# Optimization experiments

Measured on AMD Instinct MI355X. Metric: run time of the kernel, lower is better.

The kernel has to match this reference:

```python
import jax, jax.numpy as jnp
import numpy as np

D = 256   # embedding dim d; rows are d+1 = 257
N = 2048  # sequence length n; cols are n+1 = 2049
B = 16

def setup_inputs() -> dict:
    key = jax.random.key(0)
    k_h, k_p, k_q = jax.random.split(key, 3)
    H = jax.random.normal(k_h, (B, D + 1, N + 1), dtype=jnp.float32)
    P = jax.random.normal(k_p, (D + 1, D + 1), dtype=jnp.float32) * 0.01
    Q = jax.random.normal(k_q, (D + 1, D + 1), dtype=jnp.float32) * 0.01
    return {"H": H, "P": P, "Q": Q}

def reference(H, P, Q):
    # H: (B, d+1, n+1)
    n = H.shape[2] - 1
    # HtQH = H^T @ Q @ H : (B, n+1, n+1)
    HtQ = jnp.einsum('bds,de->bse', H, Q)          # (B, n+1, d+1)
    HtQH = jnp.einsum('bse,bet->bst', HtQ, H)      # (B, n+1, n+1)
    # mask M = diag(1,...,1,0): M @ HtQH zeroes the last row
    MHtQH = HtQH.at[:, -1, :].set(0.0)
    PH = jnp.einsum('de,bet->bdt', P, H)           # (B, d+1, n+1)
    attn = jnp.einsum('bds,bst->bdt', PH, MHtQH)   # (B, d+1, n+1)
    return H + attn / n
```

## Files before the change

### kernel.cpp

```cpp
#include <hip/hip_runtime.h>
#include <hip/hip_bf16.h>

#define DP     257
#define NP     2049
#define NSEQ   2048
#define NB     16
#define KLD    288
#define HROWS  320
#define TPITCH 320
#define TROWS  2176
#define KPAD   40

typedef __attribute__((ext_vector_type(8))) short bf16x8;
typedef __attribute__((ext_vector_type(4))) short bf16x4;
typedef __attribute__((ext_vector_type(4))) float f32x4;

__global__ __launch_bounds__(256) void conv_all(const float* __restrict__ H,
                                                const float* __restrict__ P,
                                                const float* __restrict__ Q,
                                                __hip_bfloat16* __restrict__ Hb,
                                                __hip_bfloat16* __restrict__ Hbt,
                                                __hip_bfloat16* __restrict__ Pb,
                                                __hip_bfloat16* __restrict__ Qt) {
    const int z  = blockIdx.z;
    const int tl = threadIdx.x & 63;
    const int er = threadIdx.x >> 6;
    __shared__ float tile[64][65];

    if (z < NB) {
        const int b  = z;
        const int t0 = blockIdx.x * 64;
        const int e0 = blockIdx.y * 64;
        const float* __restrict__ Hs = H + (size_t)b * DP * NP;
        __hip_bfloat16* __restrict__ Hbb  = Hb  + (size_t)b * HROWS * 2048;
        __hip_bfloat16* __restrict__ Hbtb = Hbt + (size_t)b * TROWS * TPITCH;

#pragma unroll
        for (int r = 0; r < 16; ++r) {
            const int el = er + r * 4;
            const int ge = e0 + el;
            const int gt = t0 + tl;
            float v = 0.f;
            if (ge < DP && gt < NP) v = Hs[(size_t)ge * NP + gt];
            tile[el][tl] = v;
            if (ge < HROWS && gt < 2048) Hbb[(size_t)ge * 2048 + gt] = __float2bfloat16(v);
        }
        __syncthreads();
#pragma unroll
        for (int r = 0; r < 16; ++r) {
            const int ttl = er + r * 4;
            const int gt = t0 + ttl;
            const int ge = e0 + tl;
            if (gt < TROWS && ge < TPITCH) {
                const float v = (ge < KLD) ? tile[tl][ttl] : 0.f;
                Hbtb[(size_t)gt * TPITCH + ge] = __float2bfloat16(v);
            }
        }
        return;
    }

    const int bx = blockIdx.x;
    if (bx >= 10) return;
    const int r0 = blockIdx.y * 64;
    if (bx < 5) {
        const int c0 = bx * 64;
#pragma unroll
        for (int r = 0; r < 16; ++r) {
            const int m = r0 + er + r * 4;
            const int k = c0 + tl;
            float v = (m < DP && k < DP) ? P[m * DP + k] : 0.f;
            if (m < KLD && k < KLD) Pb[m * KLD + k] = __float2bfloat16(v);
        }
    } else {
        const int c0 = (bx - 5) * 64;
#pragma unroll
        for (int r = 0; r < 16; ++r) {
            const int k = r0 + er + r * 4;
            const int n = c0 + tl;
            float v = (k < DP && n < DP) ? Q[k * DP + n] : 0.f;
            tile[k - r0][n - c0] = v;
        }
        __syncthreads();
#pragma unroll
        for (int r = 0; r < 16; ++r) {
            const int k = r0 + tl;
            const int n = c0 + er + r * 4;
            if (n < KLD && k < KLD) Qt[n * KLD + k] = __float2bfloat16(tile[tl][n - c0]);
        }
    }
}

__global__ __launch_bounds__(512, 4) void gram_staged(const __hip_bfloat16* __restrict__ Hb,
                                                      __hip_bfloat16* __restrict__ G) {
    const int b  = blockIdx.y;
    const int tm = blockIdx.x / 5;
    const int tn = blockIdx.x % 5;
    const int m0 = tm * 64, n0 = tn * 64;
    const int tid = threadIdx.x;
    const int wave = tid >> 6, lane = tid & 63;
    const int lrow = lane & 15, kq = (lane >> 4) * 8;
    const int hw = wave >> 2;
    const int q  = wave & 3;
    const int mh = (q & 1) * 32, nh = (q >> 1) * 32;
    const int hs = tid >> 8;
    const int t2 = tid & 255;
    const int sr = t2 >> 2;
    const int sc = (t2 & 3) * 8;

    __shared__ __align__(16) char smem[2 * 2 * 2 * 64 * KPAD * 2];
    short* As = (short*)smem;
    short* Bs = (short*)(smem + 2 * 2 * 64 * KPAD * 2);
    float* red = (float*)smem;

    const short* __restrict__ base = (const short*)(Hb + (size_t)b * HROWS * 2048);

    auto aoff = [&](int buf, int h, int r) { return ((buf * 2 + h) * 64 + r) * KPAD; };

    f32x4 acc[2][2] = {};

    {
        const int kb = hs * 1024;
        *(bf16x8*)&As[aoff(0, hs, sr) + sc] = *(const bf16x8*)(base + (size_t)(m0 + sr) * 2048 + kb + sc);
        *(bf16x8*)&Bs[aoff(0, hs, sr) + sc] = *(const bf16x8*)(base + (size_t)(n0 + sr) * 2048 + kb + sc);
    }
    __syncthreads();

    for (int kt = 0; kt < 32; ++kt) {
        const int cur = kt & 1, nxt = cur ^ 1;
        if (kt + 1 < 32) {
            const int kb = hs * 1024 + (kt + 1) * 32;
            *(bf16x8*)&As[aoff(nxt, hs, sr) + sc] = *(const bf16x8*)(base + (size_t)(m0 + sr) * 2048 + kb + sc);
            *(bf16x8*)&Bs[aoff(nxt, hs, sr) + sc] = *(const bf16x8*)(base + (size_t)(n0 + sr) * 2048 + kb + sc);
        }
        bf16x8 a0 = *(const bf16x8*)&As[aoff(cur, hw, mh + lrow) + kq];
        bf16x8 a1 = *(const bf16x8*)&As[aoff(cur, hw, mh + 16 + lrow) + kq];
        bf16x8 b0 = *(const bf16x8*)&Bs[aoff(cur, hw, nh + lrow) + kq];
        bf16x8 b1 = *(const bf16x8*)&Bs[aoff(cur, hw, nh + 16 + lrow) + kq];
        acc[0][0] = __builtin_amdgcn_mfma_f32_16x16x32_bf16(a0, b0, acc[0][0], 0, 0, 0);
        acc[0][1] = __builtin_amdgcn_mfma_f32_16x16x32_bf16(a0, b1, acc[0][1], 0, 0, 0);
        acc[1][0] = __builtin_amdgcn_mfma_f32_16x16x32_bf16(a1, b0, acc[1][0], 0, 0, 0);
        acc[1][1] = __builtin_amdgcn_mfma_f32_16x16x32_bf16(a1, b1, acc[1][1], 0, 0, 0);
        __syncthreads();
    }

    const int ccol  = lane & 15;
    const int crow0 = (lane >> 4) * 4;
#pragma unroll
    for (int i = 0; i < 2; ++i)
#pragma unroll
        for (int j = 0; j < 2; ++j)
#pragma unroll
            for (int r = 0; r < 4; ++r)
                red[((wave * 32) + i * 16 + crow0 + r) * 32 + j * 16 + ccol] = acc[i][j][r];
    __syncthreads();

    const int q2  = tid >> 7;
    const int t7  = tid & 127;
    const int row = t7 >> 2;
    const int c8  = (t7 & 3) * 8;
    const int gm = m0 + (q2 & 1) * 32 + row;
    const int gn = n0 + (q2 >> 1) * 32 + c8;
    if (gm < KLD && gn < KLD) {
        __hip_bfloat16 o[8];
#pragma unroll
        for (int t = 0; t < 8; ++t) {
            const float v = red[((q2 * 32) + row) * 32 + c8 + t] +
                            red[(((q2 + 4) * 32) + row) * 32 + c8 + t];
            o[t] = __float2bfloat16((gm < DP && (gn + t) < DP) ? v : 0.f);
        }
        __hip_bfloat16* __restrict__ Gb = G + (size_t)b * KLD * KLD;
        *(bf16x8*)&Gb[gm * KLD + gn] = *(const bf16x8*)o;
    }
}

__global__ __launch_bounds__(256) void mm_sk4(const __hip_bfloat16* __restrict__ A,
                                              const __hip_bfloat16* __restrict__ B,
                                              __hip_bfloat16* __restrict__ C,
                                              int strideA, int strideB) {
    const int b  = blockIdx.y;
    const int tm = blockIdx.x / 9;
    const int tn = blockIdx.x % 9;
    const int s    = threadIdx.x >> 6;
    const int lane = threadIdx.x & 63;
    const int lrow = lane & 15;
    const int koff = (lane >> 4) * 8;
    const short* __restrict__ Ab = (const short*)(A + (size_t)b * strideA);
    const short* __restrict__ Bb = (const short*)(B + (size_t)b * strideB);
    const int m0 = tm * 32, n0 = tn * 32;

    __shared__ float red[4][32][32];

    f32x4 acc[2][2] = {};
    for (int kt = s; kt < 9; kt += 4) {
        const int k0 = kt * 32;
        bf16x8 a0 = *(const bf16x8*)(Ab + (m0 + lrow)      * KLD + k0 + koff);
        bf16x8 a1 = *(const bf16x8*)(Ab + (m0 + 16 + lrow) * KLD + k0 + koff);
        bf16x8 c0 = *(const bf16x8*)(Bb + (n0 + lrow)      * KLD + k0 + koff);
        bf16x8 c1 = *(const bf16x8*)(Bb + (n0 + 16 + lrow) * KLD + k0 + koff);
        acc[0][0] = __builtin_amdgcn_mfma_f32_16x16x32_bf16(a0, c0, acc[0][0], 0, 0, 0);
        acc[0][1] = __builtin_amdgcn_mfma_f32_16x16x32_bf16(a0, c1, acc[0][1], 0, 0, 0);
        acc[1][0] = __builtin_amdgcn_mfma_f32_16x16x32_bf16(a1, c0, acc[1][0], 0, 0, 0);
        acc[1][1] = __builtin_amdgcn_mfma_f32_16x16x32_bf16(a1, c1, acc[1][1], 0, 0, 0);
    }

    const int ccol  = lane & 15;
    const int crow0 = (lane >> 4) * 4;
#pragma unroll
    for (int i = 0; i < 2; ++i)
#pragma unroll
        for (int j = 0; j < 2; ++j)
#pragma unroll
            for (int r = 0; r < 4; ++r)
                red[s][i * 16 + crow0 + r][j * 16 + ccol] = acc[i][j][r];
    __syncthreads();

    const int row = threadIdx.x >> 3;
    const int c4  = (threadIdx.x & 7) * 4;
    float4 v0 = *(const float4*)&red[0][row][c4];
    float4 v1 = *(const float4*)&red[1][row][c4];
    float4 v2 = *(const float4*)&red[2][row][c4];
    float4 v3 = *(const float4*)&red[3][row][c4];
    float sum[4] = {v0.x + v1.x + v2.x + v3.x,
                    v0.y + v1.y + v2.y + v3.y,
                    v0.z + v1.z + v2.z + v3.z,
                    v0.w + v1.w + v2.w + v3.w};
    const int gm = m0 + row;
    const int gn = n0 + c4;
    __hip_bfloat16 o[4];
#pragma unroll
    for (int t = 0; t < 4; ++t) {
        const float v = (gm < DP && (gn + t) < DP) ? sum[t] : 0.f;
        o[t] = __float2bfloat16(v);
    }
    __hip_bfloat16* __restrict__ Cb = C + (size_t)b * KLD * KLD;
    *(bf16x4*)&Cb[gm * KLD + gn] = *(const bf16x4*)o;
}

__global__ __launch_bounds__(256, 4) void attn_v2(const __hip_bfloat16* __restrict__ Kb,
                                                  const __hip_bfloat16* __restrict__ Hbt,
                                                  const float* __restrict__ H,
                                                  float* __restrict__ Out,
                                                  int zoff) {
    const int b  = blockIdx.z + zoff;
    const int d0 = blockIdx.y * 64;
    const int t0 = blockIdx.x * 128;
    const int tid = threadIdx.x;
    const int wave = tid >> 6, lane = tid & 63;
    const int lrow = lane & 15, kq = (lane >> 4) * 8;
    const int dh = (wave & 1) * 32;
    const int th = (wave >> 1) * 64;
    const int sr = tid >> 2;
    const int sc = (tid & 3) * 8;

    __shared__ __align__(16) char smem[(64 + 128) * KPAD * 2];
    short* As = (short*)smem;
    short* Bs = (short*)(smem + 64 * KPAD * 2);
    float* Ped = (float*)smem;

    const short* __restrict__ Ka = (const short*)(Kb  + (size_t)b * KLD * KLD);
    const short* __restrict__ Ta = (const short*)(Hbt + (size_t)b * TROWS * TPITCH);

    int rA = d0 + sr; if (rA > KLD - 1) rA = KLD - 1;

    f32x4 acc[2][4] = {};

    bf16x8 pA  = *(const bf16x8*)(Ka + (size_t)rA * KLD + sc);
    bf16x8 pB0 = *(const bf16x8*)(Ta + (size_t)(t0 + sr) * TPITCH + sc);
    bf16x8 pB1 = *(const bf16x8*)(Ta + (size_t)(t0 + 64 + sr) * TPITCH + sc);
    *(bf16x8*)&As[sr * KPAD + sc]        = pA;
    *(bf16x8*)&Bs[sr * KPAD + sc]        = pB0;
    *(bf16x8*)&Bs[(64 + sr) * KPAD + sc] = pB1;
    __syncthreads();

    for (int kt = 0; kt < 9; ++kt) {
        if (kt < 8) {
            const int e0 = (kt + 1) * 32;
            pA  = *(const bf16x8*)(Ka + (size_t)rA * KLD + e0 + sc);
            pB0 = *(const bf16x8*)(Ta + (size_t)(t0 + sr) * TPITCH + e0 + sc);
            pB1 = *(const bf16x8*)(Ta + (size_t)(t0 + 64 + sr) * TPITCH + e0 + sc);
        }
        bf16x8 af0 = *(const bf16x8*)&As[(dh + lrow) * KPAD + kq];
        bf16x8 af1 = *(const bf16x8*)&As[(dh + 16 + lrow) * KPAD + kq];
        bf16x8 bfr[4];
#pragma unroll
        for (int j = 0; j < 4; ++j)
            bfr[j] = *(const bf16x8*)&Bs[(th + j * 16 + lrow) * KPAD + kq];
#pragma unroll
        for (int j = 0; j < 4; ++j) {
            acc[0][j] = __builtin_amdgcn_mfma_f32_16x16x32_bf16(af0, bfr[j], acc[0][j], 0, 0, 0);
            acc[1][j] = __builtin_amdgcn_mfma_f32_16x16x32_bf16(af1, bfr[j], acc[1][j], 0, 0, 0);
        }
        __syncthreads();
        if (kt < 8) {
            *(bf16x8*)&As[sr * KPAD + sc]        = pA;
            *(bf16x8*)&Bs[sr * KPAD + sc]        = pB0;
            *(bf16x8*)&Bs[(64 + sr) * KPAD + sc] = pB1;
            __syncthreads();
        }
    }

    const float* __restrict__ Hs = H + (size_t)b * DP * NP;
    float* __restrict__ Ob = Out + (size_t)b * DP * NP;
    const float inv_n = 1.0f / (float)NSEQ;
    const int ccol  = lane & 15;
    const int crow0 = (lane >> 4) * 4;

#pragma unroll
    for (int c = 0; c < 4; ++c) {
        if ((wave & 1) == (c >> 1)) {
            const int i = c & 1;
#pragma unroll
            for (int j = 0; j < 4; ++j)
#pragma unroll
                for (int r = 0; r < 4; ++r)
                    Ped[(crow0 + r) * 132 + th + j * 16 + ccol] = acc[i][j][r];
        }
        __syncthreads();
#pragma unroll
        for (int p = 0; p < 2; ++p) {
            const int row = (tid >> 5) + p * 8;
            const int col = (tid & 31) * 4;
            const int gd = d0 + c * 16 + row;
            if (gd < DP) {
                const float* src = &Ped[row * 132 + col];
                const size_t base = (size_t)gd * NP;
#pragma unroll
                for (int cc = 0; cc < 4; ++cc) {
                    const int gt = t0 + col + cc;
                    if (gt < NP) {
                        const size_t idx = base + gt;
                        Ob[idx] = Hs[idx] + inv_n * src[cc];
                    }
                }
            }
        }
        __syncthreads();
    }
}

extern "C" void kernel_launch(void* const* d_in, const int* in_sizes, int n_in,
                              void* d_out, int out_size, void* d_ws, size_t ws_size,
                              hipStream_t stream) {
    const float* H = (const float*)d_in[0];
    const float* P = (const float*)d_in[1];
    const float* Q = (const float*)d_in[2];
    float* out = (float*)d_out;

    __hip_bfloat16* Hb  = (__hip_bfloat16*)d_ws;
    __hip_bfloat16* Hbt = Hb  + (size_t)NB * HROWS * 2048;
    __hip_bfloat16* G   = Hbt + (size_t)NB * TROWS * TPITCH;
    __hip_bfloat16* Pb  = G   + (size_t)NB * KLD * KLD;
    __hip_bfloat16* Qt  = Pb  + (size_t)KLD * KLD;
    __hip_bfloat16* W   = Hb;
    __hip_bfloat16* Kb  = Hb + (size_t)NB * KLD * KLD;

    conv_all<<<dim3(34, 5, NB + 1), 256, 0, stream>>>(H, P, Q, Hb, Hbt, Pb, Qt);
    gram_staged<<<dim3(25, NB), 512, 0, stream>>>(Hb, G);
    mm_sk4<<<dim3(81, NB), 256, 0, stream>>>(Pb, G, W, 0, KLD * KLD);
    mm_sk4<<<dim3(81, NB), 256, 0, stream>>>(W, Qt, Kb, KLD * KLD, 0);
    attn_v2<<<dim3(17, 5, 8), 256, 0, stream>>>(Kb, Hbt, H, out, 0);
    attn_v2<<<dim3(17, 5, 8), 256, 0, stream>>>(Kb, Hbt, H, out, 8);
}
```

Measured before the change: 188.8 us.

## Double-buffer LDS in attention GEMM, merge launches, remap blocks across XCDs

The attention kernel now uses two LDS buffers with a two-stage register prefetch, so each k-step needs one barrier instead of two. The two half-batch launches are merged into a single 1D grid. Block IDs are remapped so each group of IDs with the same value mod 8 gets a contiguous range of (batch, tile) work, which keeps K and H^T data local to one XCD's L2. This doubles LDS use per block and adds register pressure, which may lower occupancy.

```diff
diff --git a/kernel.cpp b/kernel.cpp
--- a/kernel.cpp
+++ b/kernel.cpp
@@ -236,14 +236,17 @@
     *(bf16x4*)&Cb[gm * KLD + gn] = *(const bf16x4*)o;
 }
 
-__global__ __launch_bounds__(256, 4) void attn_v2(const __hip_bfloat16* __restrict__ Kb,
+__global__ __launch_bounds__(256, 4) void attn_v5(const __hip_bfloat16* __restrict__ Kb,
                                                   const __hip_bfloat16* __restrict__ Hbt,
                                                   const float* __restrict__ H,
-                                                  float* __restrict__ Out,
-                                                  int zoff) {
-    const int b  = blockIdx.z + zoff;
-    const int d0 = blockIdx.y * 64;
-    const int t0 = blockIdx.x * 128;
+                                                  float* __restrict__ Out) {
+    const int id      = blockIdx.x;
+    const int logical = (id & 7) * 170 + (id >> 3);
+    const int b   = logical / 85;
+    const int rem = logical % 85;
+    const int t0  = (rem / 5) * 128;
+    const int d0  = (rem % 5) * 64;
+
     const int tid = threadIdx.x;
     const int wave = tid >> 6, lane = tid & 63;
     const int lrow = lane & 15, kq = (lane >> 4) * 8;
@@ -252,51 +255,64 @@
     const int sr = tid >> 2;
     const int sc = (tid & 3) * 8;
 
-    __shared__ __align__(16) char smem[(64 + 128) * KPAD * 2];
-    short* As = (short*)smem;
-    short* Bs = (short*)(smem + 64 * KPAD * 2);
-    float* Ped = (float*)smem;
+    __shared__ __align__(16) char smem[2 * (64 + 128) * KPAD * 2];
+    short* bufs = (short*)smem;
+    float* Ped  = (float*)smem;
 
     const short* __restrict__ Ka = (const short*)(Kb  + (size_t)b * KLD * KLD);
     const short* __restrict__ Ta = (const short*)(Hbt + (size_t)b * TROWS * TPITCH);
 
     int rA = d0 + sr; if (rA > KLD - 1) rA = KLD - 1;
+    const short* __restrict__ gA  = Ka + (size_t)rA * KLD + sc;
+    const short* __restrict__ gB0 = Ta + (size_t)(t0 + sr) * TPITCH + sc;
+    const short* __restrict__ gB1 = Ta + (size_t)(t0 + 64 + sr) * TPITCH + sc;
+
+    auto Aoff = [&](int bi, int r) { return (bi * 192 + r) * KPAD; };
+    auto Boff = [&](int bi, int r) { return (bi * 192 + 64 + r) * KPAD; };
 
     f32x4 acc[2][4] = {};
 
-    bf16x8 pA  = *(const bf16x8*)(Ka + (size_t)rA * KLD + sc);
-    bf16x8 pB0 = *(const bf16x8*)(Ta + (size_t)(t0 + sr) * TPITCH + sc);
-    bf16x8 pB1 = *(const bf16x8*)(Ta + (size_t)(t0 + 64 + sr) * TPITCH + sc);
-    *(bf16x8*)&As[sr * KPAD + sc]        = pA;
-    *(bf16x8*)&Bs[sr * KPAD + sc]        = pB0;
-    *(bf16x8*)&Bs[(64 + sr) * KPAD + sc] = pB1;
+    {
+        bf16x8 a = *(const bf16x8*)gA;
+        bf16x8 x = *(const bf16x8*)gB0;
+        bf16x8 y = *(const bf16x8*)gB1;
+        *(bf16x8*)&bufs[Aoff(0, sr) + sc]      = a;
+        *(bf16x8*)&bufs[Boff(0, sr) + sc]      = x;
+        *(bf16x8*)&bufs[Boff(0, 64 + sr) + sc] = y;
+    }
+    bf16x8 rA1 = *(const bf16x8*)(gA  + 32);
+    bf16x8 rB0 = *(const bf16x8*)(gB0 + 32);
+    bf16x8 rB1 = *(const bf16x8*)(gB1 + 32);
     __syncthreads();
 
+#pragma unroll
     for (int kt = 0; kt < 9; ++kt) {
-        if (kt < 8) {
-            const int e0 = (kt + 1) * 32;
-            pA  = *(const bf16x8*)(Ka + (size_t)rA * KLD + e0 + sc);
-            pB0 = *(const bf16x8*)(Ta + (size_t)(t0 + sr) * TPITCH + e0 + sc);
-            pB1 = *(const bf16x8*)(Ta + (size_t)(t0 + 64 + sr) * TPITCH + e0 + sc);
-        }
-        bf16x8 af0 = *(const bf16x8*)&As[(dh + lrow) * KPAD + kq];
-        bf16x8 af1 = *(const bf16x8*)&As[(dh + 16 + lrow) * KPAD + kq];
+        const int cur = kt & 1;
+        bf16x8 nA, nB0, nB1;
+        if (kt < 7) {
+            const int e = (kt + 2) * 32;
+            nA  = *(const bf16x8*)(gA  + e);
+            nB0 = *(const bf16x8*)(gB0 + e);
+            nB1 = *(const bf16x8*)(gB1 + e);
+        }
+        bf16x8 af0 = *(const bf16x8*)&bufs[Aoff(cur, dh + lrow) + kq];
+        bf16x8 af1 = *(const bf16x8*)&bufs[Aoff(cur, dh + 16 + lrow) + kq];
         bf16x8 bfr[4];
 #pragma unroll
         for (int j = 0; j < 4; ++j)
-            bfr[j] = *(const bf16x8*)&Bs[(th + j * 16 + lrow) * KPAD + kq];
+            bfr[j] = *(const bf16x8*)&bufs[Boff(cur, th + j * 16 + lrow) + kq];
 #pragma unroll
         for (int j = 0; j < 4; ++j) {
             acc[0][j] = __builtin_amdgcn_mfma_f32_16x16x32_bf16(af0, bfr[j], acc[0][j], 0, 0, 0);
             acc[1][j] = __builtin_amdgcn_mfma_f32_16x16x32_bf16(af1, bfr[j], acc[1][j], 0, 0, 0);
         }
-        __syncthreads();
         if (kt < 8) {
-            *(bf16x8*)&As[sr * KPAD + sc]        = pA;
-            *(bf16x8*)&Bs[sr * KPAD + sc]        = pB0;
-            *(bf16x8*)&Bs[(64 + sr) * KPAD + sc] = pB1;
-            __syncthreads();
-        }
+            *(bf16x8*)&bufs[Aoff(cur ^ 1, sr) + sc]      = rA1;
+            *(bf16x8*)&bufs[Boff(cur ^ 1, sr) + sc]      = rB0;
+            *(bf16x8*)&bufs[Boff(cur ^ 1, 64 + sr) + sc] = rB1;
+        }
+        __syncthreads();
+        if (kt < 7) { rA1 = nA; rB0 = nB0; rB1 = nB1; }
     }
 
     const float* __restrict__ Hs = H + (size_t)b * DP * NP;
@@ -358,6 +374,5 @@
     gram_staged<<<dim3(25, NB), 512, 0, stream>>>(Hb, G);
     mm_sk4<<<dim3(81, NB), 256, 0, stream>>>(Pb, G, W, 0, KLD * KLD);
     mm_sk4<<<dim3(81, NB), 256, 0, stream>>>(W, Qt, Kb, KLD * KLD, 0);
-    attn_v2<<<dim3(17, 5, 8), 256, 0, stream>>>(Kb, Hbt, H, out, 0);
-    attn_v2<<<dim3(17, 5, 8), 256, 0, stream>>>(Kb, Hbt, H, out, 8);
-}
+    attn_v5<<<dim3(17 * 5 * NB), 256, 0, stream>>>(Kb, Hbt, H, out);
+}
```

After: 173.7 us. -8.0%, faster.
